# Optimization experiments

Hardware: AMD Instinct MI355X
Metric: run time of the kernel (lower is better)

## Reference

```python
import jax, jax.numpy as jnp
import numpy as np

# Static problem sizes (must match input construction)
B, G, EPG, K, C = 64, 24, 512, 20, 1
NS = B * G            # total number of subgraphs
E = NS * EPG          # total number of edges
M, H = 4096, 256      # node_state shape


def setup_inputs() -> dict:
    key = jax.random.key(0)
    ks = jax.random.split(key, 8)
    label = (jax.random.uniform(ks[0], (E,)) < 0.5).astype(jnp.float32)
    label0 = (jax.random.uniform(ks[1], (E,)) < 0.5).astype(jnp.float32)
    log_theta = jax.random.normal(ks[2], (E, K), dtype=jnp.float32)
    log_theta0 = jax.random.normal(ks[3], (E, K), dtype=jnp.float32)
    log_alpha = jax.random.normal(ks[4], (E, K), dtype=jnp.float32)
    log_alpha0 = jax.random.normal(ks[5], (E, K), dtype=jnp.float32)
    subgraph_idx = (jnp.arange(E, dtype=jnp.int32) // EPG).astype(jnp.int32)
    subgraph_idx0 = subgraph_idx
    subgraph_idx_base = (jnp.arange(B + 1, dtype=jnp.int32) * (G * C)).astype(jnp.int32)
    subgraph_idx_base0 = subgraph_idx_base
    node_state = jax.random.normal(ks[6], (M, H), dtype=jnp.float32)
    node_state0 = jax.random.normal(ks[7], (M, H), dtype=jnp.float32)
    return {
        "label": label, "label0": label0,
        "log_theta": log_theta, "log_theta0": log_theta0,
        "log_alpha": log_alpha, "log_alpha0": log_alpha0,
        "subgraph_idx": subgraph_idx, "subgraph_idx0": subgraph_idx0,
        "subgraph_idx_base": subgraph_idx_base, "subgraph_idx_base0": subgraph_idx_base0,
        "node_state": node_state, "node_state0": node_state0,
    }


def _bce_with_logits(logits, y):
    # BCEWithLogitsLoss(reduction='none'), broadcast label over K mixture components
    return -(y[:, None] * jax.nn.log_sigmoid(logits)
             + (1.0 - y)[:, None] * jax.nn.log_sigmoid(-logits))


def _stream_loss(label, log_theta, log_alpha, subgraph_idx, subgraph_idx_base):
    adj_loss = _bce_with_logits(log_theta, label)                     # E x K
    const = jax.ops.segment_sum(jnp.ones((E,), jnp.float32), subgraph_idx, NS)  # edges per subgraph
    reduce_adj_loss = jax.ops.segment_sum(adj_loss, subgraph_idx, NS)  # NS x K
    reduce_log_alpha = jax.ops.segment_sum(log_alpha, subgraph_idx, NS) / const[:, None]
    reduce_log_alpha = jax.nn.log_softmax(reduce_log_alpha, axis=-1)
    log_prob = jax.nn.logsumexp(-reduce_adj_loss + reduce_log_alpha, axis=1)  # NS
    # bc_idx: map each subgraph to its (batch, canonical-order) slot; C == 1 here,
    # equivalent to repeat_interleave(arange(B*C), bc_size) in the original.
    bc_idx = jnp.searchsorted(subgraph_idx_base, jnp.arange(NS, dtype=jnp.int32), side='right') - 1
    bc_log_prob = jax.ops.segment_sum(log_prob, bc_idx, B * C).reshape(B, C)
    bc_const = jax.ops.segment_sum(const, bc_idx, B * C).reshape(B, C)
    bc_loss = bc_log_prob / bc_const
    b_loss = jax.nn.logsumexp(bc_loss, axis=1)   # sum_order_log_prob=False
    return jnp.mean(-b_loss)                      # reduction='mean'


def _trace_cdist(ns, ns0):
    # Fused replacement for the naive O(m^2) host-side pairwise-distance loop:
    # D[i,j] = ||ns[i] - ns0[j]||, then trace(D).
    x2 = jnp.sum(ns * ns, axis=1)
    y2 = jnp.sum(ns0 * ns0, axis=1)
    d2 = x2[:, None] + y2[None, :] - 2.0 * (ns @ ns0.T)   # M x M
    D = jnp.sqrt(jnp.maximum(d2, 0.0))
    return jnp.trace(D)


def reference(label, label0, log_theta, log_theta0, log_alpha, log_alpha0,
              subgraph_idx, subgraph_idx0, subgraph_idx_base, subgraph_idx_base0,
              node_state, node_state0):
    loss = _stream_loss(label, log_theta, log_alpha, subgraph_idx, subgraph_idx_base)
    loss0 = _stream_loss(label0, log_theta0, log_alpha0, subgraph_idx0, subgraph_idx_base0)
    trD = _trace_cdist(node_state, node_state0)
    # return_neg_log_prob=False branch of the original
    return 10.0 * (loss + loss0) + trD
```

## Files before the change

### kernel.cpp

```cpp
#include <hip/hip_runtime.h>
#include <math.h>

#define B_   64
#define G_   24
#define EPG_ 512
#define K_   20
#define NS_  (B_ * G_)
#define E_   (NS_ * EPG_)
#define M_   4096
#define H_   256
#define F4_  (EPG_ * K_ / 4)

#define NB1_ 1536
#define NT1_ 320
#define T1_  (NB1_ * NT1_)
#define NV_  8
#define SPV_ (T1_ / F4_)

#define CD_ROWS_   20
#define CD_BLOCKS_ ((M_ + CD_ROWS_ - 1) / CD_ROWS_)

#define WS_FLOATS_ (2 * 2 * NS_ * K_)

__device__ __forceinline__ float bce_f(float x, float y) {
    return fmaxf(x, 0.f) - x * y + __logf(1.f + __expf(-fabsf(x)));
}

__global__ __launch_bounds__(NT1_)
void accum_kernel(const float* __restrict__ label,
                  const float* __restrict__ label0,
                  const float4* __restrict__ gt,
                  const float4* __restrict__ gt0,
                  const float4* __restrict__ ga,
                  const float4* __restrict__ ga0,
                  const float* __restrict__ ns,
                  const float* __restrict__ ns0,
                  float* __restrict__ ws,
                  float* __restrict__ out)
{
    __shared__ float4 s_red[4][NT1_];
    __shared__ float  s_cd[5];

    const int tid = threadIdx.x;

    if (blockIdx.x >= NB1_) {
        const int cb = blockIdx.x - NB1_;
        const int wave = tid >> 6, lane = tid & 63;
        float acc = 0.f;
        #pragma unroll
        for (int i = 0; i < 4; ++i) {
            const int row = cb * CD_ROWS_ + wave * 4 + i;
            if (row < M_) {
                const float4 a = ((const float4*)(ns  + (size_t)row * H_))[lane];
                const float4 b = ((const float4*)(ns0 + (size_t)row * H_))[lane];
                const float dx = a.x - b.x, dy = a.y - b.y;
                const float dz = a.z - b.z, dw = a.w - b.w;
                float sv = dx * dx + dy * dy + dz * dz + dw * dw;
                #pragma unroll
                for (int off = 32; off > 0; off >>= 1) sv += __shfl_down(sv, off);
                if (lane == 0) acc += sqrtf(sv);
            }
        }
        if (lane == 0) s_cd[wave] = acc;
        __syncthreads();
        if (tid == 0)
            atomicAdd(out, s_cd[0] + s_cd[1] + s_cd[2] + s_cd[3] + s_cd[4]);
        return;
    }

    const int b    = blockIdx.x;
    const int sgrp = b >> 3;

    const int g   = tid >> 2, sub = tid & 3;
    const int qt  = g / 20,  k   = g % 20;
    const int q   = k >> 2,  j   = k & 3;
    const float* basep = (const float*)&s_red[qt][0];
    const int ws_base = (((qt >> 1) * 2 + (qt & 1)) * NS_) * K_ + k;

    {
        const size_t f = (size_t)b * NT1_ + tid;
        const int    e = b * 64 + tid / 5;
        float4 x0 = gt[f], x1 = gt0[f], c0 = ga[f], c1 = ga0[f];
        float  y0 = label[e], y1 = label0[e];

        for (int v = 0; v < NV_; ++v) {
            float4 nx0, nx1, nc0, nc1; float ny0, ny1;
            if (v + 1 < NV_) {
                const size_t fn = (size_t)(v + 1) * T1_ + (size_t)b * NT1_ + tid;
                const int    en = (v + 1) * (T1_ / 5) + b * 64 + tid / 5;
                nx0 = gt[fn]; nx1 = gt0[fn]; nc0 = ga[fn]; nc1 = ga0[fn];
                ny0 = label[en]; ny1 = label0[en];
            }

            float4 J0, J1;
            J0.x = bce_f(x0.x, y0); J0.y = bce_f(x0.y, y0);
            J0.z = bce_f(x0.z, y0); J0.w = bce_f(x0.w, y0);
            J1.x = bce_f(x1.x, y1); J1.y = bce_f(x1.y, y1);
            J1.z = bce_f(x1.z, y1); J1.w = bce_f(x1.w, y1);
            s_red[0][tid] = J0;  s_red[1][tid] = J1;
            s_red[2][tid] = c0;  s_red[3][tid] = c1;
            __syncthreads();

            {
                float vsum = 0.f;
                #pragma unroll
                for (int mm = 0; mm < 16; ++mm)
                    vsum += basep[(q + 20 * mm + 5 * sub) * 4 + j];
                vsum += __shfl_down(vsum, 2);
                vsum += __shfl_down(vsum, 1);
                if (sub == 0) {
                    const int s = v * SPV_ + sgrp;
                    atomicAdd(&ws[ws_base + s * K_], vsum);
                }
            }
            __syncthreads();

            x0 = nx0; x1 = nx1; c0 = nc0; c1 = nc1; y0 = ny0; y1 = ny1;
        }
    }
}

__global__ __launch_bounds__(256)
void finish_kernel(const float* __restrict__ ws, float* __restrict__ out)
{
    const int gid = blockIdx.x * 256 + threadIdx.x;
    const int st = gid & 1, s = gid >> 1;
    const float* Wadj = ws + ((0 * 2 + st) * NS_ + s) * K_;
    const float* Walp = ws + ((1 * 2 + st) * NS_ + s) * K_;

    const float inv_c = 1.0f / (float)EPG_;
    float va[K_];
    #pragma unroll
    for (int kk = 0; kk < K_; ++kk) va[kk] = Walp[kk] * inv_c;
    float m1 = -INFINITY;
    #pragma unroll
    for (int kk = 0; kk < K_; ++kk) m1 = fmaxf(m1, va[kk]);
    float s1 = 0.f;
    #pragma unroll
    for (int kk = 0; kk < K_; ++kk) s1 += __expf(va[kk] - m1);
    const float lse = m1 + __logf(s1);

    float w[K_];
    float m2 = -INFINITY;
    #pragma unroll
    for (int kk = 0; kk < K_; ++kk) {
        w[kk] = va[kk] - lse - Wadj[kk];
        m2 = fmaxf(m2, w[kk]);
    }
    float s2 = 0.f;
    #pragma unroll
    for (int kk = 0; kk < K_; ++kk) s2 += __expf(w[kk] - m2);
    const float lp = m2 + __logf(s2);

    atomicAdd(out, lp * (-10.0f / (float)E_));
}

extern "C" void kernel_launch(void* const* d_in, const int* in_sizes, int n_in,
                              void* d_out, int out_size, void* d_ws, size_t ws_size,
                              hipStream_t stream) {
    const float* label       = (const float*)d_in[0];
    const float* label0      = (const float*)d_in[1];
    const float* log_theta   = (const float*)d_in[2];
    const float* log_theta0  = (const float*)d_in[3];
    const float* log_alpha   = (const float*)d_in[4];
    const float* log_alpha0  = (const float*)d_in[5];
    const float* node_state  = (const float*)d_in[10];
    const float* node_state0 = (const float*)d_in[11];
    float* out = (float*)d_out;
    float* ws  = (float*)d_ws;

    hipMemsetAsync(out, 0, sizeof(float), stream);
    hipMemsetAsync(ws, 0, WS_FLOATS_ * sizeof(float), stream);

    accum_kernel<<<dim3(NB1_ + CD_BLOCKS_), NT1_, 0, stream>>>(
        label, label0,
        (const float4*)log_theta, (const float4*)log_theta0,
        (const float4*)log_alpha, (const float4*)log_alpha0,
        node_state, node_state0, ws, out);

    finish_kernel<<<dim3(12), 256, 0, stream>>>(ws, out);
}
```

Measured before the change: 272.3 us.

## Accumulate per-subgraph sums in registers and reduce with shuffles, dropping shared memory

Restructures the loss sweep so each of 320 threads per subgraph walks that subgraph's edges in a strided loop. Partial BCE and alpha sums stay in registers, then a cross-lane shuffle reduction with strides that are multiples of 5 produces one value per K component, followed by a few atomics per wave. This replaces the per-iteration shared-memory staging, the two block barriers per iteration and the per-block atomics. It also splits the trace-distance rows into 16-row blocks of 256 threads. The trade-off is more register pressure and less explicit prefetching, and correctness depends on the lane-to-component mapping within each wave.

```diff
diff --git a/kernel.cpp b/kernel.cpp
--- a/kernel.cpp
+++ b/kernel.cpp
@@ -11,14 +11,10 @@
 #define H_   256
 #define F4_  (EPG_ * K_ / 4)
 
-#define NB1_ 1536
-#define NT1_ 320
-#define T1_  (NB1_ * NT1_)
-#define NV_  8
-#define SPV_ (T1_ / F4_)
-
-#define CD_ROWS_   20
-#define CD_BLOCKS_ ((M_ + CD_ROWS_ - 1) / CD_ROWS_)
+#define TPS_ 320
+#define NIT_ (F4_ / TPS_)
+#define NB_LOSS_ (NS_ * TPS_ / 256)
+#define CD_BLOCKS_ (M_ / 16)
 
 #define WS_FLOATS_ (2 * 2 * NS_ * K_)
 
@@ -26,8 +22,20 @@
     return fmaxf(x, 0.f) - x * y + __logf(1.f + __expf(-fabsf(x)));
 }
 
-__global__ __launch_bounds__(NT1_)
-void accum_kernel(const float* __restrict__ label,
+__device__ __forceinline__ void cls_reduce(float4& v, int lane) {
+    #pragma unroll
+    for (int d = 40; d >= 5; d >>= 1) {
+        float4 t;
+        t.x = __shfl(v.x, lane + d);
+        t.y = __shfl(v.y, lane + d);
+        t.z = __shfl(v.z, lane + d);
+        t.w = __shfl(v.w, lane + d);
+        if (lane + d < 64) { v.x += t.x; v.y += t.y; v.z += t.z; v.w += t.w; }
+    }
+}
+
+__global__ __launch_bounds__(256, 8)
+void sweep_kernel(const float* __restrict__ label,
                   const float* __restrict__ label0,
                   const float4* __restrict__ gt,
                   const float4* __restrict__ gt0,
@@ -38,85 +46,77 @@
                   float* __restrict__ ws,
                   float* __restrict__ out)
 {
-    __shared__ float4 s_red[4][NT1_];
-    __shared__ float  s_cd[5];
-
     const int tid = threadIdx.x;
 
-    if (blockIdx.x >= NB1_) {
-        const int cb = blockIdx.x - NB1_;
+    if (blockIdx.x >= NB_LOSS_) {
+        __shared__ float s_d[16];
+        const int cb = blockIdx.x - NB_LOSS_;
         const int wave = tid >> 6, lane = tid & 63;
-        float acc = 0.f;
         #pragma unroll
         for (int i = 0; i < 4; ++i) {
-            const int row = cb * CD_ROWS_ + wave * 4 + i;
-            if (row < M_) {
-                const float4 a = ((const float4*)(ns  + (size_t)row * H_))[lane];
-                const float4 b = ((const float4*)(ns0 + (size_t)row * H_))[lane];
-                const float dx = a.x - b.x, dy = a.y - b.y;
-                const float dz = a.z - b.z, dw = a.w - b.w;
-                float sv = dx * dx + dy * dy + dz * dz + dw * dw;
-                #pragma unroll
-                for (int off = 32; off > 0; off >>= 1) sv += __shfl_down(sv, off);
-                if (lane == 0) acc += sqrtf(sv);
-            }
+            const int row = cb * 16 + wave * 4 + i;
+            const float4 a = ((const float4*)(ns  + (size_t)row * H_))[lane];
+            const float4 b = ((const float4*)(ns0 + (size_t)row * H_))[lane];
+            const float dx = a.x - b.x, dy = a.y - b.y;
+            const float dz = a.z - b.z, dw = a.w - b.w;
+            float sv = dx * dx + dy * dy + dz * dz + dw * dw;
+            #pragma unroll
+            for (int off = 32; off > 0; off >>= 1) sv += __shfl_down(sv, off);
+            if (lane == 0) s_d[wave * 4 + i] = sqrtf(sv);
         }
-        if (lane == 0) s_cd[wave] = acc;
         __syncthreads();
-        if (tid == 0)
-            atomicAdd(out, s_cd[0] + s_cd[1] + s_cd[2] + s_cd[3] + s_cd[4]);
+        if (tid == 0) {
+            float t = 0.f;
+            #pragma unroll
+            for (int i = 0; i < 16; ++i) t += s_d[i];
+            atomicAdd(out, t);
+        }
         return;
     }
 
-    const int b    = blockIdx.x;
-    const int sgrp = b >> 3;
+    const int n = blockIdx.x * 256 + tid;
+    const int s = n / TPS_, u = n % TPS_;
+    const int f0 = s * F4_ + u;
+    const int e0 = s * EPG_ + u / 5;
 
-    const int g   = tid >> 2, sub = tid & 3;
-    const int qt  = g / 20,  k   = g % 20;
-    const int q   = k >> 2,  j   = k & 3;
-    const float* basep = (const float*)&s_red[qt][0];
-    const int ws_base = (((qt >> 1) * 2 + (qt & 1)) * NS_) * K_ + k;
+    float4 J0 = {0,0,0,0}, J1 = {0,0,0,0}, A0 = {0,0,0,0}, A1 = {0,0,0,0};
 
-    {
-        const size_t f = (size_t)b * NT1_ + tid;
-        const int    e = b * 64 + tid / 5;
-        float4 x0 = gt[f], x1 = gt0[f], c0 = ga[f], c1 = ga0[f];
-        float  y0 = label[e], y1 = label0[e];
+    #pragma unroll
+    for (int i = 0; i < NIT_; ++i) {
+        const int f = f0 + i * TPS_;
+        const float  y0 = label[e0 + i * 64];
+        const float  y1 = label0[e0 + i * 64];
+        const float4 x0 = gt[f], x1 = gt0[f], c0 = ga[f], c1 = ga0[f];
+        J0.x += bce_f(x0.x, y0); J0.y += bce_f(x0.y, y0);
+        J0.z += bce_f(x0.z, y0); J0.w += bce_f(x0.w, y0);
+        J1.x += bce_f(x1.x, y1); J1.y += bce_f(x1.y, y1);
+        J1.z += bce_f(x1.z, y1); J1.w += bce_f(x1.w, y1);
+        A0.x += c0.x; A0.y += c0.y; A0.z += c0.z; A0.w += c0.w;
+        A1.x += c1.x; A1.y += c1.y; A1.z += c1.z; A1.w += c1.w;
+    }
 
-        for (int v = 0; v < NV_; ++v) {
-            float4 nx0, nx1, nc0, nc1; float ny0, ny1;
-            if (v + 1 < NV_) {
-                const size_t fn = (size_t)(v + 1) * T1_ + (size_t)b * NT1_ + tid;
-                const int    en = (v + 1) * (T1_ / 5) + b * 64 + tid / 5;
-                nx0 = gt[fn]; nx1 = gt0[fn]; nc0 = ga[fn]; nc1 = ga0[fn];
-                ny0 = label[en]; ny1 = label0[en];
-            }
+    const int lane = tid & 63;
+    cls_reduce(J0, lane);
+    cls_reduce(J1, lane);
+    cls_reduce(A0, lane);
+    cls_reduce(A1, lane);
 
-            float4 J0, J1;
-            J0.x = bce_f(x0.x, y0); J0.y = bce_f(x0.y, y0);
-            J0.z = bce_f(x0.z, y0); J0.w = bce_f(x0.w, y0);
-            J1.x = bce_f(x1.x, y1); J1.y = bce_f(x1.y, y1);
-            J1.z = bce_f(x1.z, y1); J1.w = bce_f(x1.w, y1);
-            s_red[0][tid] = J0;  s_red[1][tid] = J1;
-            s_red[2][tid] = c0;  s_red[3][tid] = c1;
-            __syncthreads();
-
-            {
-                float vsum = 0.f;
-                #pragma unroll
-                for (int mm = 0; mm < 16; ++mm)
-                    vsum += basep[(q + 20 * mm + 5 * sub) * 4 + j];
-                vsum += __shfl_down(vsum, 2);
-                vsum += __shfl_down(vsum, 1);
-                if (sub == 0) {
-                    const int s = v * SPV_ + sgrp;
-                    atomicAdd(&ws[ws_base + s * K_], vsum);
-                }
-            }
-            __syncthreads();
-
-            x0 = nx0; x1 = nx1; c0 = nc0; c1 = nc1; y0 = ny0; y1 = ny1;
-        }
+    if (lane < 5) {
+        const int u0 = u - lane;
+        const int q  = (u0 + lane) % 5;
+        const int kb = 4 * q;
+        float* w00 = ws + ((0 * 2 + 0) * NS_ + s) * K_ + kb;
+        float* w01 = ws + ((0 * 2 + 1) * NS_ + s) * K_ + kb;
+        float* w10 = ws + ((1 * 2 + 0) * NS_ + s) * K_ + kb;
+        float* w11 = ws + ((1 * 2 + 1) * NS_ + s) * K_ + kb;
+        atomicAdd(w00 + 0, J0.x); atomicAdd(w00 + 1, J0.y);
+        atomicAdd(w00 + 2, J0.z); atomicAdd(w00 + 3, J0.w);
+        atomicAdd(w01 + 0, J1.x); atomicAdd(w01 + 1, J1.y);
+        atomicAdd(w01 + 2, J1.z); atomicAdd(w01 + 3, J1.w);
+        atomicAdd(w10 + 0, A0.x); atomicAdd(w10 + 1, A0.y);
+        atomicAdd(w10 + 2, A0.z); atomicAdd(w10 + 3, A0.w);
+        atomicAdd(w11 + 0, A1.x); atomicAdd(w11 + 1, A1.y);
+        atomicAdd(w11 + 2, A1.z); atomicAdd(w11 + 3, A1.w);
     }
 }
 
@@ -172,7 +172,7 @@
     hipMemsetAsync(out, 0, sizeof(float), stream);
     hipMemsetAsync(ws, 0, WS_FLOATS_ * sizeof(float), stream);
 
-    accum_kernel<<<dim3(NB1_ + CD_BLOCKS_), NT1_, 0, stream>>>(
+    sweep_kernel<<<dim3(NB_LOSS_ + CD_BLOCKS_), 256, 0, stream>>>(
         label, label0,
         (const float4*)log_theta, (const float4*)log_theta0,
         (const float4*)log_alpha, (const float4*)log_alpha0,
```

New measurement: 325.0 us. +19.4%, slower.
